# Kernel optimization log

Hardware: AMD Instinct MI355X
Metric: run time of the kernel (lower is better)

Reference implementation:

```python
import jax, jax.numpy as jnp
import numpy as np

N_NODES = 10000
N_EDGES = 320000


def setup_inputs() -> dict:
    key = jax.random.key(0)
    ks = jax.random.split(key, 8)
    node_features = jax.random.normal(ks[0], (N_NODES, 128), dtype=jnp.float32)
    edge_src = jax.random.randint(ks[1], (N_EDGES,), 0, N_NODES, dtype=jnp.int32)
    edge_dst = jax.random.randint(ks[2], (N_EDGES,), 0, N_NODES, dtype=jnp.int32)
    # QCNN params: Linear(128->256)+Tanh, Linear(256->256)+Tanh, then sigmoid; out Linear(256->128)
    W1 = jax.random.normal(ks[3], (128, 256), dtype=jnp.float32) / np.sqrt(128)
    b1 = jnp.zeros((256,), dtype=jnp.float32)
    W2 = jax.random.normal(ks[4], (256, 256), dtype=jnp.float32) / np.sqrt(256)
    b2 = jnp.zeros((256,), dtype=jnp.float32)
    Wo = jax.random.normal(ks[5], (256, 128), dtype=jnp.float32) / np.sqrt(256)
    bo = jnp.zeros((128,), dtype=jnp.float32)
    return dict(node_features=node_features, edge_src=edge_src, edge_dst=edge_dst,
                W1=W1, b1=b1, W2=W2, b2=b2, Wo=Wo, bo=bo)


def reference(node_features, edge_src, edge_dst, W1, b1, W2, b2, Wo, bo):
    # QCNN dense encoder: tanh MLP followed by sigmoid
    h = jnp.tanh(node_features @ W1 + b1)        # [N, 256]
    h = jnp.tanh(h @ W2 + b2)                    # [N, 256]
    hidden = jax.nn.sigmoid(h)                   # [N, 256]
    # Neighbor mean aggregation (segment mean over incoming edges).
    # Nodes with no neighbors keep zeros, matching the torch loop.
    sums = jax.ops.segment_sum(hidden[edge_src], edge_dst, num_segments=N_NODES)  # [N, 256]
    deg = jax.ops.segment_sum(jnp.ones_like(edge_dst, dtype=hidden.dtype), edge_dst,
                              num_segments=N_NODES)                              # [N]
    agg = sums / jnp.maximum(deg, 1.0)[:, None]
    return agg @ Wo + bo                         # [N, 128]
```

## Files before the change

kernel.cpp:

```cpp
#include <hip/hip_runtime.h>
#include <hip/hip_bf16.h>

#define NN 10000
#define NE 320000

typedef __attribute__((ext_vector_type(8))) short bf16x8;
typedef __attribute__((ext_vector_type(4))) float f32x4;
typedef __attribute__((ext_vector_type(8))) unsigned short ushort8;

__device__ inline void split_bf16(float a, unsigned short& hi, unsigned short& lo) {
  union { float f; unsigned int u; } v; v.f = a;
  hi = (unsigned short)(v.u >> 16);
  union { float f; unsigned int u; } h; h.u = (unsigned int)hi << 16;
  float r = a - h.f;
  union { float f; unsigned int u; } w; w.f = r;
  lo = (unsigned short)(w.u >> 16);
}

__global__ __launch_bounds__(256) void prep_kernel(
    const float* __restrict__ X, unsigned short* __restrict__ Xhi,
    unsigned short* __restrict__ Xlo,
    const float* __restrict__ W1, unsigned short* __restrict__ W1thi,
    unsigned short* __restrict__ W1tlo,
    const float* __restrict__ W2, unsigned short* __restrict__ W2thi,
    unsigned short* __restrict__ W2tlo,
    const float* __restrict__ Wo, unsigned short* __restrict__ Wothi,
    unsigned short* __restrict__ Wotlo,
    int* __restrict__ deg) {
  int i = blockIdx.x * 256 + threadIdx.x;

  if (i < 2500) ((int4*)deg)[i] = make_int4(0, 0, 0, 0);

  {
    float4 x = ((const float4*)X)[i];
    ushort4 h, l;
    split_bf16(x.x, h.x, l.x);
    split_bf16(x.y, h.y, l.y);
    split_bf16(x.z, h.z, l.z);
    split_bf16(x.w, h.w, l.w);
    ((ushort4*)Xhi)[i] = h;
    ((ushort4*)Xlo)[i] = l;
  }

  if (i < 32768) {
    int n = i >> 7, k = i & 127;
    unsigned short h, l; split_bf16(W1[k * 256 + n], h, l);
    W1thi[i] = h; W1tlo[i] = l;
  }
  if (i < 65536) {
    int n = i >> 8, k = i & 255;
    unsigned short h, l; split_bf16(W2[k * 256 + n], h, l);
    W2thi[i] = h; W2tlo[i] = l;
  }
  if (i >= 65536 && i < 98304) {
    int o = i - 65536;
    int n = o >> 8, k = o & 255;
    unsigned short h, l; split_bf16(Wo[k * 128 + n], h, l);
    Wothi[o] = h; Wotlo[o] = l;
  }
}

template<int ACT, bool BIAS_, int OUTM, int K, int N>
__global__ __launch_bounds__(256) void mfma_gemm(
    const unsigned short* __restrict__ Ahi_g, const unsigned short* __restrict__ Alo_g,
    const unsigned short* __restrict__ Bthi_g, const unsigned short* __restrict__ Btlo_g,
    const float* __restrict__ bias, float* __restrict__ Cf,
    unsigned short* __restrict__ Chi, unsigned short* __restrict__ Clo, int M) {
  __shared__ unsigned short Ah[64 * 64], Al[64 * 64], Bh[64 * 64], Bl[64 * 64];

  const int tid = threadIdx.x;
  const int lane = tid & 63;
  const int wid = tid >> 6;
  const int wr = wid >> 1, wc = wid & 1;
  const int row0 = blockIdx.x * 64;
  const int col0 = blockIdx.y * 64;

  f32x4 acc[2][2];
#pragma unroll
  for (int m = 0; m < 2; m++)
#pragma unroll
    for (int n = 0; n < 2; n++) acc[m][n] = (f32x4){0.f, 0.f, 0.f, 0.f};

  for (int kt = 0; kt < K / 64; ++kt) {
#pragma unroll
    for (int it = 0; it < 2; ++it) {
      int c = it * 256 + tid;
      int r = c >> 3, cj = c & 7;
      int dj = (cj ^ (r & 7)) * 8;
      int grow = row0 + r; if (grow > M - 1) grow = M - 1;
      size_t ga = (size_t)grow * K + kt * 64 + cj * 8;
      *(ushort8*)&Ah[r * 64 + dj] = *(const ushort8*)&Ahi_g[ga];
      *(ushort8*)&Al[r * 64 + dj] = *(const ushort8*)&Alo_g[ga];
      size_t gb = (size_t)(col0 + r) * K + kt * 64 + cj * 8;
      *(ushort8*)&Bh[r * 64 + dj] = *(const ushort8*)&Bthi_g[gb];
      *(ushort8*)&Bl[r * 64 + dj] = *(const ushort8*)&Btlo_g[gb];
    }
    __syncthreads();
#pragma unroll
    for (int kk = 0; kk < 2; ++kk) {
      bf16x8 aH[2], aL[2], bH[2], bL[2];
#pragma unroll
      for (int m = 0; m < 2; m++) {
        int row = wr * 32 + m * 16 + (lane & 15);
        int ch = (kk * 4 + (lane >> 4)) ^ (row & 7);
        aH[m] = *(const bf16x8*)&Ah[row * 64 + ch * 8];
        aL[m] = *(const bf16x8*)&Al[row * 64 + ch * 8];
      }
#pragma unroll
      for (int n = 0; n < 2; n++) {
        int col = wc * 32 + n * 16 + (lane & 15);
        int ch = (kk * 4 + (lane >> 4)) ^ (col & 7);
        bH[n] = *(const bf16x8*)&Bh[col * 64 + ch * 8];
        bL[n] = *(const bf16x8*)&Bl[col * 64 + ch * 8];
      }
#pragma unroll
      for (int m = 0; m < 2; m++)
#pragma unroll
        for (int n = 0; n < 2; n++) {
          acc[m][n] = __builtin_amdgcn_mfma_f32_16x16x32_bf16(aH[m], bH[n], acc[m][n], 0, 0, 0);
          acc[m][n] = __builtin_amdgcn_mfma_f32_16x16x32_bf16(aH[m], bL[n], acc[m][n], 0, 0, 0);
          acc[m][n] = __builtin_amdgcn_mfma_f32_16x16x32_bf16(aL[m], bH[n], acc[m][n], 0, 0, 0);
        }
    }
    __syncthreads();
  }

#pragma unroll
  for (int m = 0; m < 2; m++)
#pragma unroll
    for (int n = 0; n < 2; n++) {
      int col = col0 + wc * 32 + n * 16 + (lane & 15);
      float bv = BIAS_ ? bias[col] : 0.f;
#pragma unroll
      for (int j = 0; j < 4; j++) {
        int row = row0 + wr * 32 + m * 16 + (lane >> 4) * 4 + j;
        if (row < M) {
          float v = acc[m][n][j] + bv;
          if (ACT == 1) v = tanhf(v);
          else if (ACT == 2) v = 1.f / (1.f + expf(-tanhf(v)));
          if (OUTM == 0) {
            Cf[(size_t)row * N + col] = v;
          } else {
            unsigned short h, l; split_bf16(v, h, l);
            Chi[(size_t)row * N + col] = h;
            Clo[(size_t)row * N + col] = l;
          }
        }
      }
    }
}

__global__ void count_kernel(const int* __restrict__ dst, int* __restrict__ deg, int n) {
  int i = blockIdx.x * blockDim.x + threadIdx.x;
  if (i < n) atomicAdd(&deg[dst[i]], 1);
}

__global__ __launch_bounds__(1024) void scan_kernel(
    const int* __restrict__ deg, int* __restrict__ offs, int* __restrict__ cursor) {
  __shared__ int wsum[16];
  int t = threadIdx.x;
  int base = t * 10;
  int loc[10];
  int s = 0;
  if (base < NN) {
#pragma unroll
    for (int i = 0; i < 10; i++) {
      int idx = base + i;
      int v = (idx < NN) ? deg[idx] : 0;
      loc[i] = s; s += v;
    }
  }
  int lane = t & 63, w = t >> 6;
  int incl = s;
  for (int off = 1; off < 64; off <<= 1) {
    int u = __shfl_up(incl, off, 64);
    if (lane >= off) incl += u;
  }
  if (lane == 63) wsum[w] = incl;
  __syncthreads();
  if (t == 0) {
    int c = 0;
#pragma unroll
    for (int i = 0; i < 16; i++) { int v = wsum[i]; wsum[i] = c; c += v; }
  }
  __syncthreads();
  int ex = wsum[w] + incl - s;
  if (base < NN) {
#pragma unroll
    for (int i = 0; i < 10; i++) {
      int idx = base + i;
      if (idx < NN) { int o = ex + loc[i]; offs[idx] = o; cursor[idx] = o; }
    }
  }
}

__global__ void fill_kernel(const int* __restrict__ src, const int* __restrict__ dst,
                            int* __restrict__ cursor, int* __restrict__ csr, int n) {
  int i = blockIdx.x * blockDim.x + threadIdx.x;
  if (i < n) {
    int d = dst[i];
    int pos = atomicAdd(&cursor[d], 1);
    csr[pos] = src[i];
  }
}

__global__ __launch_bounds__(256) void aggregate_kernel(
    const float* __restrict__ hproj, const int* __restrict__ csr,
    const int* __restrict__ offs, const int* __restrict__ deg,
    const float* __restrict__ bo, float* __restrict__ out, int n_nodes) {
  int wave = threadIdx.x >> 6;
  int lane = threadIdx.x & 63;
  int node = blockIdx.x * 4 + wave;
  if (node >= n_nodes) return;
  int start = offs[node];
  int d = deg[node];
  const float2* h2 = (const float2*)hproj;
  float2 acc0 = make_float2(0.f, 0.f), acc1 = make_float2(0.f, 0.f);
  for (int t0 = 0; t0 < d; t0 += 64) {
    int rem = d - t0; if (rem > 64) rem = 64;
    int idx = (lane < rem) ? csr[start + t0 + lane] : 0;
    int j = 0;
    for (; j + 8 <= rem; j += 8) {
      int s0 = __shfl(idx, j + 0), s1 = __shfl(idx, j + 1);
      int s2 = __shfl(idx, j + 2), s3 = __shfl(idx, j + 3);
      int s4 = __shfl(idx, j + 4), s5 = __shfl(idx, j + 5);
      int s6 = __shfl(idx, j + 6), s7 = __shfl(idx, j + 7);
      float2 v0 = h2[s0 * 64 + lane], v1 = h2[s1 * 64 + lane];
      float2 v2 = h2[s2 * 64 + lane], v3 = h2[s3 * 64 + lane];
      float2 v4 = h2[s4 * 64 + lane], v5 = h2[s5 * 64 + lane];
      float2 v6 = h2[s6 * 64 + lane], v7 = h2[s7 * 64 + lane];
      acc0.x += (v0.x + v1.x) + (v2.x + v3.x);
      acc0.y += (v0.y + v1.y) + (v2.y + v3.y);
      acc1.x += (v4.x + v5.x) + (v6.x + v7.x);
      acc1.y += (v4.y + v5.y) + (v6.y + v7.y);
    }
    for (; j < rem; j++) {
      int s = __shfl(idx, j);
      float2 v = h2[s * 64 + lane];
      acc0.x += v.x; acc0.y += v.y;
    }
  }
  float scale = 1.f / fmaxf((float)d, 1.f);
  float2 b = ((const float2*)bo)[lane];
  float2 o;
  o.x = fmaf(acc0.x + acc1.x, scale, b.x);
  o.y = fmaf(acc0.y + acc1.y, scale, b.y);
  ((float2*)out)[node * 64 + lane] = o;
}

extern "C" void kernel_launch(void* const* d_in, const int* in_sizes, int n_in,
                              void* d_out, int out_size, void* d_ws, size_t ws_size,
                              hipStream_t stream) {
  const float* X    = (const float*)d_in[0];
  const int*   esrc = (const int*)d_in[1];
  const int*   edst = (const int*)d_in[2];
  const float* W1   = (const float*)d_in[3];
  const float* b1   = (const float*)d_in[4];
  const float* W2   = (const float*)d_in[5];
  const float* b2   = (const float*)d_in[6];
  const float* Wo   = (const float*)d_in[7];
  const float* bo   = (const float*)d_in[8];
  float* out = (float*)d_out;

  char* p = (char*)d_ws;
  size_t needed = (size_t)NN * 256 * 4 * 2
                + (size_t)(32768 + 65536 + 32768) * 2 * 2
                + (size_t)(3 * NN + NE) * 4;
  if (ws_size < needed) return;

  unsigned short* regA  = (unsigned short*)p;
  unsigned short* Xhi   = regA;
  unsigned short* Xlo   = regA + (size_t)NN * 128;
  unsigned short* hidhi = regA;
  unsigned short* hidlo = regA + (size_t)NN * 256;
  p += (size_t)NN * 256 * 4;
  unsigned short* h1hi  = (unsigned short*)p;
  unsigned short* h1lo  = h1hi + (size_t)NN * 256;
  float*          hproj = (float*)h1hi;
  p += (size_t)NN * 256 * 4;
  unsigned short* W1thi = (unsigned short*)p; p += 32768 * 2;
  unsigned short* W1tlo = (unsigned short*)p; p += 32768 * 2;
  unsigned short* W2thi = (unsigned short*)p; p += 65536 * 2;
  unsigned short* W2tlo = (unsigned short*)p; p += 65536 * 2;
  unsigned short* Wothi = (unsigned short*)p; p += 32768 * 2;
  unsigned short* Wotlo = (unsigned short*)p; p += 32768 * 2;
  int* deg    = (int*)p; p += (size_t)NN * 4;
  int* offs   = (int*)p; p += (size_t)NN * 4;
  int* cursor = (int*)p; p += (size_t)NN * 4;
  int* csr    = (int*)p; p += (size_t)NE * 4;

  prep_kernel<<<1250, 256, 0, stream>>>(X, Xhi, Xlo, W1, W1thi, W1tlo,
                                        W2, W2thi, W2tlo, Wo, Wothi, Wotlo, deg);

  count_kernel<<<(NE + 255) / 256, 256, 0, stream>>>(edst, deg, NE);
  scan_kernel<<<1, 1024, 0, stream>>>(deg, offs, cursor);
  fill_kernel<<<(NE + 255) / 256, 256, 0, stream>>>(esrc, edst, cursor, csr, NE);

  mfma_gemm<1, true, 1, 128, 256><<<dim3(157, 4), 256, 0, stream>>>(
      Xhi, Xlo, W1thi, W1tlo, b1, nullptr, h1hi, h1lo, NN);
  mfma_gemm<2, true, 1, 256, 256><<<dim3(157, 4), 256, 0, stream>>>(
      h1hi, h1lo, W2thi, W2tlo, b2, nullptr, hidhi, hidlo, NN);
  mfma_gemm<0, false, 0, 256, 128><<<dim3(157, 2), 256, 0, stream>>>(
      hidhi, hidlo, Wothi, Wotlo, nullptr, hproj, nullptr, nullptr, NN);

  aggregate_kernel<<<(NN + 3) / 4, 256, 0, stream>>>(hproj, csr, offs, deg, bo, out, NN);
}
```

Baseline: 174.6 us.

## Fuse three MLP GEMMs into one row-tile kernel with LDS-resident activations

```diff
diff --git a/kernel.cpp b/kernel.cpp
--- a/kernel.cpp
+++ b/kernel.cpp
@@ -3,12 +3,13 @@
 
 #define NN 10000
 #define NE 320000
+#define MLP_BLOCKS 157
 
 typedef __attribute__((ext_vector_type(8))) short bf16x8;
 typedef __attribute__((ext_vector_type(4))) float f32x4;
 typedef __attribute__((ext_vector_type(8))) unsigned short ushort8;
 
-__device__ inline void split_bf16(float a, unsigned short& hi, unsigned short& lo) {
+__device__ __forceinline__ void split_bf16(float a, unsigned short& hi, unsigned short& lo) {
   union { float f; unsigned int u; } v; v.f = a;
   hi = (unsigned short)(v.u >> 16);
   union { float f; unsigned int u; } h; h.u = (unsigned int)hi << 16;
@@ -18,30 +19,12 @@
 }
 
 __global__ __launch_bounds__(256) void prep_kernel(
-    const float* __restrict__ X, unsigned short* __restrict__ Xhi,
-    unsigned short* __restrict__ Xlo,
-    const float* __restrict__ W1, unsigned short* __restrict__ W1thi,
-    unsigned short* __restrict__ W1tlo,
-    const float* __restrict__ W2, unsigned short* __restrict__ W2thi,
-    unsigned short* __restrict__ W2tlo,
-    const float* __restrict__ Wo, unsigned short* __restrict__ Wothi,
-    unsigned short* __restrict__ Wotlo,
+    const float* __restrict__ W1, unsigned short* __restrict__ W1thi, unsigned short* __restrict__ W1tlo,
+    const float* __restrict__ W2, unsigned short* __restrict__ W2thi, unsigned short* __restrict__ W2tlo,
+    const float* __restrict__ Wo, unsigned short* __restrict__ Wothi, unsigned short* __restrict__ Wotlo,
     int* __restrict__ deg) {
   int i = blockIdx.x * 256 + threadIdx.x;
-
   if (i < 2500) ((int4*)deg)[i] = make_int4(0, 0, 0, 0);
-
-  {
-    float4 x = ((const float4*)X)[i];
-    ushort4 h, l;
-    split_bf16(x.x, h.x, l.x);
-    split_bf16(x.y, h.y, l.y);
-    split_bf16(x.z, h.z, l.z);
-    split_bf16(x.w, h.w, l.w);
-    ((ushort4*)Xhi)[i] = h;
-    ((ushort4*)Xlo)[i] = l;
-  }
-
   if (i < 32768) {
     int n = i >> 7, k = i & 127;
     unsigned short h, l; split_bf16(W1[k * 256 + n], h, l);
@@ -52,7 +35,7 @@
     unsigned short h, l; split_bf16(W2[k * 256 + n], h, l);
     W2thi[i] = h; W2tlo[i] = l;
   }
-  if (i >= 65536 && i < 98304) {
+  if (i >= 65536) {
     int o = i - 65536;
     int n = o >> 8, k = o & 255;
     unsigned short h, l; split_bf16(Wo[k * 128 + n], h, l);
@@ -60,99 +43,142 @@
   }
 }
 
-template<int ACT, bool BIAS_, int OUTM, int K, int N>
-__global__ __launch_bounds__(256) void mfma_gemm(
-    const unsigned short* __restrict__ Ahi_g, const unsigned short* __restrict__ Alo_g,
-    const unsigned short* __restrict__ Bthi_g, const unsigned short* __restrict__ Btlo_g,
-    const float* __restrict__ bias, float* __restrict__ Cf,
-    unsigned short* __restrict__ Chi, unsigned short* __restrict__ Clo, int M) {
-  __shared__ unsigned short Ah[64 * 64], Al[64 * 64], Bh[64 * 64], Bl[64 * 64];
-
-  const int tid = threadIdx.x;
-  const int lane = tid & 63;
-  const int wid = tid >> 6;
-  const int wr = wid >> 1, wc = wid & 1;
+template<int K, int NFRAG>
+__device__ __forceinline__ void layer_mfma(
+    const unsigned short* Ah, const unsigned short* Al,
+    const unsigned short* __restrict__ Bthi, const unsigned short* __restrict__ Btlo,
+    int lane, int colbase, f32x4 (&acc)[4][NFRAG]) {
+  const int l15 = lane & 15, l16 = lane >> 4;
+#pragma unroll
+  for (int m = 0; m < 4; m++)
+#pragma unroll
+    for (int n = 0; n < NFRAG; n++) acc[m][n] = (f32x4){0.f, 0.f, 0.f, 0.f};
+#pragma unroll 2
+  for (int kk = 0; kk < K / 32; ++kk) {
+    bf16x8 aH[4], aL[4], bH[NFRAG], bL[NFRAG];
+#pragma unroll
+    for (int m = 0; m < 4; m++) {
+      int r = m * 16 + l15;
+      int c = (kk * 4 + l16) ^ (r & 7);
+      aH[m] = *(const bf16x8*)&Ah[r * 256 + c * 8];
+      aL[m] = *(const bf16x8*)&Al[r * 256 + c * 8];
+    }
+#pragma unroll
+    for (int n = 0; n < NFRAG; n++) {
+      int col = colbase + n * 16 + l15;
+      size_t off = (size_t)col * K + kk * 32 + l16 * 8;
+      bH[n] = *(const bf16x8*)&Bthi[off];
+      bL[n] = *(const bf16x8*)&Btlo[off];
+    }
+#pragma unroll
+    for (int m = 0; m < 4; m++)
+#pragma unroll
+      for (int n = 0; n < NFRAG; n++) {
+        acc[m][n] = __builtin_amdgcn_mfma_f32_16x16x32_bf16(aH[m], bH[n], acc[m][n], 0, 0, 0);
+        acc[m][n] = __builtin_amdgcn_mfma_f32_16x16x32_bf16(aH[m], bL[n], acc[m][n], 0, 0, 0);
+        acc[m][n] = __builtin_amdgcn_mfma_f32_16x16x32_bf16(aL[m], bH[n], acc[m][n], 0, 0, 0);
+      }
+  }
+}
+
+template<int ACT>
+__device__ __forceinline__ void writeback_lds(
+    unsigned short* Ah, unsigned short* Al, f32x4 (&acc)[4][4],
+    const float* __restrict__ bias, int lane, int colbase) {
+  const int l15 = lane & 15, l16 = lane >> 4;
+#pragma unroll
+  for (int n = 0; n < 4; n++) {
+    int col = colbase + n * 16 + l15;
+    float bv = bias[col];
+#pragma unroll
+    for (int m = 0; m < 4; m++)
+#pragma unroll
+      for (int j = 0; j < 4; j++) {
+        int r = m * 16 + l16 * 4 + j;
+        float v = acc[m][n][j] + bv;
+        if (ACT == 1) v = tanhf(v);
+        else v = 1.f / (1.f + expf(-tanhf(v)));
+        unsigned short h, l; split_bf16(v, h, l);
+        int c = col >> 3, e = col & 7;
+        int idx = r * 256 + ((c ^ (r & 7)) * 8) + e;
+        Ah[idx] = h; Al[idx] = l;
+      }
+  }
+}
+
+__global__ __launch_bounds__(256) void mega_kernel(
+    const float* __restrict__ X,
+    const unsigned short* __restrict__ W1thi, const unsigned short* __restrict__ W1tlo,
+    const float* __restrict__ b1,
+    const unsigned short* __restrict__ W2thi, const unsigned short* __restrict__ W2tlo,
+    const float* __restrict__ b2,
+    const unsigned short* __restrict__ Wothi, const unsigned short* __restrict__ Wotlo,
+    float* __restrict__ hproj,
+    const int* __restrict__ edst, int* __restrict__ deg) {
+  if (blockIdx.x >= MLP_BLOCKS) {
+    int e = (blockIdx.x - MLP_BLOCKS) * 256 + threadIdx.x;
+    if (e < NE) atomicAdd(&deg[edst[e]], 1);
+    return;
+  }
+  __shared__ unsigned short Ah[64 * 256], Al[64 * 256];
+  const int tid = threadIdx.x, lane = tid & 63, w = tid >> 6;
   const int row0 = blockIdx.x * 64;
-  const int col0 = blockIdx.y * 64;
-
-  f32x4 acc[2][2];
-#pragma unroll
-  for (int m = 0; m < 2; m++)
-#pragma unroll
-    for (int n = 0; n < 2; n++) acc[m][n] = (f32x4){0.f, 0.f, 0.f, 0.f};
-
-  for (int kt = 0; kt < K / 64; ++kt) {
-#pragma unroll
-    for (int it = 0; it < 2; ++it) {
-      int c = it * 256 + tid;
-      int r = c >> 3, cj = c & 7;
-      int dj = (cj ^ (r & 7)) * 8;
-      int grow = row0 + r; if (grow > M - 1) grow = M - 1;
-      size_t ga = (size_t)grow * K + kt * 64 + cj * 8;
-      *(ushort8*)&Ah[r * 64 + dj] = *(const ushort8*)&Ahi_g[ga];
-      *(ushort8*)&Al[r * 64 + dj] = *(const ushort8*)&Alo_g[ga];
-      size_t gb = (size_t)(col0 + r) * K + kt * 64 + cj * 8;
-      *(ushort8*)&Bh[r * 64 + dj] = *(const ushort8*)&Bthi_g[gb];
-      *(ushort8*)&Bl[r * 64 + dj] = *(const ushort8*)&Btlo_g[gb];
-    }
+
+#pragma unroll
+  for (int it = 0; it < 4; ++it) {
+    int slot = it * 256 + tid;
+    int r = slot >> 4, c = slot & 15;
+    int gr = row0 + r; if (gr > NN - 1) gr = NN - 1;
+    const float* xp = &X[(size_t)gr * 128 + c * 8];
+    float4 x0 = *(const float4*)xp;
+    float4 x1 = *(const float4*)(xp + 4);
+    unsigned short h0, l0, h1, l1, h2, l2, h3, l3;
+    unsigned short h4, l4, h5, l5, h6, l6, h7, l7;
+    split_bf16(x0.x, h0, l0); split_bf16(x0.y, h1, l1);
+    split_bf16(x0.z, h2, l2); split_bf16(x0.w, h3, l3);
+    split_bf16(x1.x, h4, l4); split_bf16(x1.y, h5, l5);
+    split_bf16(x1.z, h6, l6); split_bf16(x1.w, h7, l7);
+    ushort8 h, l;
+    h[0] = h0; h[1] = h1; h[2] = h2; h[3] = h3;
+    h[4] = h4; h[5] = h5; h[6] = h6; h[7] = h7;
+    l[0] = l0; l[1] = l1; l[2] = l2; l[3] = l3;
+    l[4] = l4; l[5] = l5; l[6] = l6; l[7] = l7;
+    int base = r * 256 + ((c ^ (r & 7)) * 8);
+    *(ushort8*)&Ah[base] = h;
+    *(ushort8*)&Al[base] = l;
+  }
+  __syncthreads();
+
+  {
+    f32x4 acc[4][4];
+    layer_mfma<128, 4>(Ah, Al, W1thi, W1tlo, lane, w * 64, acc);
     __syncthreads();
-#pragma unroll
-    for (int kk = 0; kk < 2; ++kk) {
-      bf16x8 aH[2], aL[2], bH[2], bL[2];
-#pragma unroll
-      for (int m = 0; m < 2; m++) {
-        int row = wr * 32 + m * 16 + (lane & 15);
-        int ch = (kk * 4 + (lane >> 4)) ^ (row & 7);
-        aH[m] = *(const bf16x8*)&Ah[row * 64 + ch * 8];
-        aL[m] = *(const bf16x8*)&Al[row * 64 + ch * 8];
-      }
-#pragma unroll
-      for (int n = 0; n < 2; n++) {
-        int col = wc * 32 + n * 16 + (lane & 15);
-        int ch = (kk * 4 + (lane >> 4)) ^ (col & 7);
-        bH[n] = *(const bf16x8*)&Bh[col * 64 + ch * 8];
-        bL[n] = *(const bf16x8*)&Bl[col * 64 + ch * 8];
-      }
-#pragma unroll
-      for (int m = 0; m < 2; m++)
-#pragma unroll
-        for (int n = 0; n < 2; n++) {
-          acc[m][n] = __builtin_amdgcn_mfma_f32_16x16x32_bf16(aH[m], bH[n], acc[m][n], 0, 0, 0);
-          acc[m][n] = __builtin_amdgcn_mfma_f32_16x16x32_bf16(aH[m], bL[n], acc[m][n], 0, 0, 0);
-          acc[m][n] = __builtin_amdgcn_mfma_f32_16x16x32_bf16(aL[m], bH[n], acc[m][n], 0, 0, 0);
+    writeback_lds<1>(Ah, Al, acc, b1, lane, w * 64);
+    __syncthreads();
+  }
+  {
+    f32x4 acc[4][4];
+    layer_mfma<256, 4>(Ah, Al, W2thi, W2tlo, lane, w * 64, acc);
+    __syncthreads();
+    writeback_lds<2>(Ah, Al, acc, b2, lane, w * 64);
+    __syncthreads();
+  }
+  {
+    f32x4 acc[4][2];
+    layer_mfma<256, 2>(Ah, Al, Wothi, Wotlo, lane, w * 32, acc);
+    const int l15 = lane & 15, l16 = lane >> 4;
+#pragma unroll
+    for (int n = 0; n < 2; n++) {
+      int col = w * 32 + n * 16 + l15;
+#pragma unroll
+      for (int m = 0; m < 4; m++)
+#pragma unroll
+        for (int j = 0; j < 4; j++) {
+          int grow = row0 + m * 16 + l16 * 4 + j;
+          if (grow < NN) hproj[(size_t)grow * 128 + col] = acc[m][n][j];
         }
     }
-    __syncthreads();
-  }
-
-#pragma unroll
-  for (int m = 0; m < 2; m++)
-#pragma unroll
-    for (int n = 0; n < 2; n++) {
-      int col = col0 + wc * 32 + n * 16 + (lane & 15);
-      float bv = BIAS_ ? bias[col] : 0.f;
-#pragma unroll
-      for (int j = 0; j < 4; j++) {
-        int row = row0 + wr * 32 + m * 16 + (lane >> 4) * 4 + j;
-        if (row < M) {
-          float v = acc[m][n][j] + bv;
-          if (ACT == 1) v = tanhf(v);
-          else if (ACT == 2) v = 1.f / (1.f + expf(-tanhf(v)));
-          if (OUTM == 0) {
-            Cf[(size_t)row * N + col] = v;
-          } else {
-            unsigned short h, l; split_bf16(v, h, l);
-            Chi[(size_t)row * N + col] = h;
-            Clo[(size_t)row * N + col] = l;
-          }
-        }
-      }
-    }
-}
-
-__global__ void count_kernel(const int* __restrict__ dst, int* __restrict__ deg, int n) {
-  int i = blockIdx.x * blockDim.x + threadIdx.x;
-  if (i < n) atomicAdd(&deg[dst[i]], 1);
+  }
 }
 
 __global__ __launch_bounds__(1024) void scan_kernel(
@@ -263,21 +289,12 @@
   float* out = (float*)d_out;
 
   char* p = (char*)d_ws;
-  size_t needed = (size_t)NN * 256 * 4 * 2
+  size_t needed = (size_t)NN * 128 * 4
                 + (size_t)(32768 + 65536 + 32768) * 2 * 2
                 + (size_t)(3 * NN + NE) * 4;
   if (ws_size < needed) return;
 
-  unsigned short* regA  = (unsigned short*)p;
-  unsigned short* Xhi   = regA;
-  unsigned short* Xlo   = regA + (size_t)NN * 128;
-  unsigned short* hidhi = regA;
-  unsigned short* hidlo = regA + (size_t)NN * 256;
-  p += (size_t)NN * 256 * 4;
-  unsigned short* h1hi  = (unsigned short*)p;
-  unsigned short* h1lo  = h1hi + (size_t)NN * 256;
-  float*          hproj = (float*)h1hi;
-  p += (size_t)NN * 256 * 4;
+  float* hproj = (float*)p;                   p += (size_t)NN * 128 * 4;
   unsigned short* W1thi = (unsigned short*)p; p += 32768 * 2;
   unsigned short* W1tlo = (unsigned short*)p; p += 32768 * 2;
   unsigned short* W2thi = (unsigned short*)p; p += 65536 * 2;
@@ -289,19 +306,11 @@
   int* cursor = (int*)p; p += (size_t)NN * 4;
   int* csr    = (int*)p; p += (size_t)NE * 4;
 
-  prep_kernel<<<1250, 256, 0, stream>>>(X, Xhi, Xlo, W1, W1thi, W1tlo,
-                                        W2, W2thi, W2tlo, Wo, Wothi, Wotlo, deg);
-
-  count_kernel<<<(NE + 255) / 256, 256, 0, stream>>>(edst, deg, NE);
+  prep_kernel<<<384, 256, 0, stream>>>(W1, W1thi, W1tlo, W2, W2thi, W2tlo,
+                                       Wo, Wothi, Wotlo, deg);
+  mega_kernel<<<MLP_BLOCKS + (NE + 255) / 256, 256, 0, stream>>>(
+      X, W1thi, W1tlo, b1, W2thi, W2tlo, b2, Wothi, Wotlo, hproj, edst, deg);
   scan_kernel<<<1, 1024, 0, stream>>>(deg, offs, cursor);
   fill_kernel<<<(NE + 255) / 256, 256, 0, stream>>>(esrc, edst, cursor, csr, NE);
-
-  mfma_gemm<1, true, 1, 128, 256><<<dim3(157, 4), 256, 0, stream>>>(
-      Xhi, Xlo, W1thi, W1tlo, b1, nullptr, h1hi, h1lo, NN);
-  mfma_gemm<2, true, 1, 256, 256><<<dim3(157, 4), 256, 0, stream>>>(
-      h1hi, h1lo, W2thi, W2tlo, b2, nullptr, hidhi, hidlo, NN);
-  mfma_gemm<0, false, 0, 256, 128><<<dim3(157, 2), 256, 0, stream>>>(
-      hidhi, hidlo, Wothi, Wotlo, nullptr, hproj, nullptr, nullptr, NN);
-
   aggregate_kernel<<<(NN + 3) / 4, 256, 0, stream>>>(hproj, csr, offs, deg, bo, out, NN);
 }
```

Measured after the change: 155.6 us. 10.9% less time.
